# Kernel optimization log

Measured on AMD Instinct MI355X. Metric: run time of the kernel, lower is better.

Reference implementation:

```python
import math
import jax, jax.numpy as jnp
import numpy as np

H, KV, D = 16, 4, 128          # num_heads, num_kv_heads, head_dim
HID = 2048                      # hidden_size
ROPE_BASE = 1e6
EPS = 1e-6


def setup_inputs() -> dict:
    key = jax.random.key(0)
    ks = jax.random.split(key, 3)
    B, S = 2, 2048
    s = 0.02
    return {
        "x": jax.random.normal(ks[0], (B, S, HID), jnp.float32),
        "w_qkv": jax.random.normal(ks[1], (2 * H * D + 2 * KV * D, HID), jnp.float32) * s,
        "w_o": jax.random.normal(ks[2], (HID, H * D), jnp.float32) * s,
        "q_norm_w": jnp.ones((D,), jnp.float32),
        "q_norm_b": jnp.zeros((D,), jnp.float32),
        "k_norm_w": jnp.ones((D,), jnp.float32),
        "k_norm_b": jnp.zeros((D,), jnp.float32),
    }


def _layernorm(x, w, b):
    mu = jnp.mean(x, axis=-1, keepdims=True)
    xc = x - mu
    var = jnp.mean(xc * xc, axis=-1, keepdims=True)
    return xc * jax.lax.rsqrt(var + EPS) * w + b


def _rope(x, cos, sin):
    # x: [B, h, S, D]; cos/sin: [S, D/2]; interleaved real/imag pairs
    xr, xi = x[..., 0::2], x[..., 1::2]
    c, s = cos[None, None], sin[None, None]
    out = jnp.stack([xr * c - xi * s, xr * s + xi * c], axis=-1)
    return out.reshape(x.shape)


def reference(x, w_qkv, w_o, q_norm_w, q_norm_b, k_norm_w, k_norm_b):
    B, S, _ = x.shape
    qkv = x @ w_qkv.T                                  # [B,S,2*H*D+2*KV*D]
    qg, k, v = jnp.split(qkv, [2 * H * D, 2 * H * D + KV * D], axis=-1)
    q, gate = jnp.split(qg, 2, axis=-1)                # [B,S,H*D] each

    q = q.reshape(B, S, H, D).transpose(0, 2, 1, 3)    # [B,H,S,D]
    k = k.reshape(B, S, KV, D).transpose(0, 2, 1, 3)   # [B,KV,S,D]
    v = v.reshape(B, S, KV, D).transpose(0, 2, 1, 3)

    q = _layernorm(q, q_norm_w, q_norm_b)
    k = _layernorm(k, k_norm_w, k_norm_b)

    inv = 1.0 / (ROPE_BASE ** (jnp.arange(0, D, 2, dtype=jnp.float32) / D))
    freqs = jnp.outer(jnp.arange(S, dtype=jnp.float32), inv)  # [S, D/2]
    cos, sin = jnp.cos(freqs), jnp.sin(freqs)
    q = _rope(q, cos, sin)
    k = _rope(k, cos, sin)

    rep = H // KV
    k = jnp.repeat(k, rep, axis=1)                     # [B,H,S,D]
    v = jnp.repeat(v, rep, axis=1)

    scores = jnp.einsum('bhqd,bhkd->bhqk', q, k) / math.sqrt(D)
    causal = jnp.tril(jnp.ones((S, S), bool))
    scores = jnp.where(causal[None, None], scores, -jnp.inf)
    attn = jax.nn.softmax(scores, axis=-1)
    out = jnp.einsum('bhqk,bhkd->bhqd', attn, v)
    out = out.transpose(0, 2, 1, 3).reshape(B, S, H * D)
    out = out * jax.nn.sigmoid(gate)
    return out @ w_o.T
```

## Files before the change

kernel.cpp:

```cpp
#include <hip/hip_runtime.h>
#include <hip/hip_bf16.h>

typedef __bf16 bf16_t;
typedef __bf16 bf16x2 __attribute__((ext_vector_type(2)));
typedef __bf16 bf16x4v __attribute__((ext_vector_type(4)));
typedef __bf16 bf16x8 __attribute__((ext_vector_type(8)));
typedef float f32x4 __attribute__((ext_vector_type(4)));

#define LOG2E 1.4426950408889634f
#define QSCALE (0.08838834764831843f * 1.4426950408889634f)

__global__ __launch_bounds__(256) void cvt_all(const float* __restrict__ x, bf16_t* __restrict__ xb,
                                               const float* __restrict__ wq, bf16_t* __restrict__ wqb,
                                               const float* __restrict__ wo, bf16_t* __restrict__ wob,
                                               float* __restrict__ cosT, float* __restrict__ sinT) {
  int i = blockIdx.x * 256 + threadIdx.x;
  if (i < 5767168) {
    const float* in; bf16_t* out; int idx;
    if (i < 2097152)      { in = x;  out = xb;  idx = i; }
    else if (i < 4718592) { in = wq; out = wqb; idx = i - 2097152; }
    else                  { in = wo; out = wob; idx = i - 4718592; }
    float4 v = ((const float4*)in)[idx];
    bf16x4v o;
    o[0] = (__bf16)v.x; o[1] = (__bf16)v.y; o[2] = (__bf16)v.z; o[3] = (__bf16)v.w;
    *(bf16x4v*)(out + (size_t)idx * 4) = o;
  } else {
    int idx = i - 5767168;
    int s = idx >> 6, fi = idx & 63;
    float inv = __builtin_amdgcn_exp2f(-(float)fi * (19.931568569324174f / 64.0f));
    float f = (float)s * inv;
    cosT[idx] = cosf(f);
    sinT[idx] = sinf(f);
  }
}

template<int MI, int NI, typename OT>
__global__ __launch_bounds__(512) void gemm8p(const bf16_t* __restrict__ A,
                                              const bf16_t* __restrict__ B,
                                              OT* __restrict__ C,
                                              int M, int N, int K) {
  constexpr int BM = MI * 32;
  constexpr int BN = NI * 64;
  constexpr int NA = BM / 64;
  constexpr int NB = BN / 64;
  constexpr int ST = NA + NB;
  static_assert(MI == 8 || MI == 4, "banked phases assume MI in {4,8}");

  __shared__ bf16_t LA[2][BM * 64];
  __shared__ bf16_t LB[2][BN * 64];

  int nb = N / BN;
  int cpx = gridDim.x >> 3;
  int bid = blockIdx.x;
  int swz = (bid & 7) * cpx + (bid >> 3);
  int bm = swz / nb, bn = swz % nb;
  int m0 = bm * BM, n0 = bn * BN;
  int tid = threadIdx.x, lane = tid & 63, wv = tid >> 6;
  int wr = wv >> 2, wc = wv & 3, lr = lane & 15, g = lane >> 4;
  int T = K >> 6;

  auto stageI = [&](int kt, int bi, int s) {
    int k0 = kt << 6;
    if (s < NA) {
      int c = s * 512 + tid;
      int row = c >> 3, lc = (c & 7) ^ (row & 7);
      __builtin_amdgcn_global_load_lds(
          (const __attribute__((address_space(1))) void*)(A + (size_t)(m0 + row) * K + k0 + lc * 8),
          (__attribute__((address_space(3))) void*)&LA[bi][(s * 512 + wv * 64) * 8], 16, 0, 0);
    } else {
      int c = (s - NA) * 512 + tid;
      int row = c >> 3, lc = (c & 7) ^ (row & 7);
      __builtin_amdgcn_global_load_lds(
          (const __attribute__((address_space(1))) void*)(B + (size_t)(n0 + row) * K + k0 + lc * 8),
          (__attribute__((address_space(3))) void*)&LB[bi][((s - NA) * 512 + wv * 64) * 8], 16, 0, 0);
    }
  };

  f32x4 acc[MI][NI];
#pragma unroll
  for (int i = 0; i < MI; i++)
#pragma unroll
    for (int j = 0; j < NI; j++)
#pragma unroll
      for (int r = 0; r < 4; r++) acc[i][j][r] = 0.f;

#pragma unroll
  for (int s = 0; s < ST; s++) stageI(0, 0, s);
  asm volatile("s_waitcnt vmcnt(0)" ::: "memory");
  __builtin_amdgcn_s_barrier();
  asm volatile("" ::: "memory");

  int ofk0 = ((0 + g) ^ (lr & 7)) << 3;
  int ofk1 = ((4 + g) ^ (lr & 7)) << 3;
  int offA = (wr * (MI * 16) + lr) * 64;
  int offB = (wc * (NI * 16) + lr) * 64;

  for (int t = 0; t < T; t++) {
    int bi = t & 1, bo = bi ^ 1;
    const bf16_t* la = LA[bi];
    const bf16_t* lb = LB[bi];
    bool pre = (t + 1 < T);
    if (pre) {
#pragma unroll
      for (int s = 0; s < ST; s++) stageI(t + 1, bo, s);
    }

    bf16x8 bq0[NI], bq1[NI], afA[4], afB[4];
#pragma unroll
    for (int ni = 0; ni < NI; ni++) bq0[ni] = *(const bf16x8*)&lb[offB + ni * 1024 + ofk0];
#pragma unroll
    for (int i = 0; i < 4; i++) afA[i] = *(const bf16x8*)&la[offA + i * 1024 + ofk0];

    if constexpr (MI == 8) {
#pragma unroll
      for (int i = 0; i < 4; i++) afB[i] = *(const bf16x8*)&la[offA + (4 + i) * 1024 + ofk0];
#pragma unroll
      for (int i = 0; i < 4; i++)
#pragma unroll
        for (int ni = 0; ni < NI; ni++)
          acc[i][ni] = __builtin_amdgcn_mfma_f32_16x16x32_bf16(afA[i], bq0[ni], acc[i][ni], 0, 0, 0);
#pragma unroll
      for (int i = 0; i < 4; i++) afA[i] = *(const bf16x8*)&la[offA + i * 1024 + ofk1];
#pragma unroll
      for (int ni = 0; ni < NI; ni++) bq1[ni] = *(const bf16x8*)&lb[offB + ni * 1024 + ofk1];
#pragma unroll
      for (int i = 0; i < 4; i++)
#pragma unroll
        for (int ni = 0; ni < NI; ni++)
          acc[4 + i][ni] = __builtin_amdgcn_mfma_f32_16x16x32_bf16(afB[i], bq0[ni], acc[4 + i][ni], 0, 0, 0);
#pragma unroll
      for (int i = 0; i < 4; i++) afB[i] = *(const bf16x8*)&la[offA + (4 + i) * 1024 + ofk1];
#pragma unroll
      for (int i = 0; i < 4; i++)
#pragma unroll
        for (int ni = 0; ni < NI; ni++)
          acc[i][ni] = __builtin_amdgcn_mfma_f32_16x16x32_bf16(afA[i], bq1[ni], acc[i][ni], 0, 0, 0);
#pragma unroll
      for (int i = 0; i < 4; i++)
#pragma unroll
        for (int ni = 0; ni < NI; ni++)
          acc[4 + i][ni] = __builtin_amdgcn_mfma_f32_16x16x32_bf16(afB[i], bq1[ni], acc[4 + i][ni], 0, 0, 0);
    } else {
#pragma unroll
      for (int i = 0; i < 4; i++) afB[i] = *(const bf16x8*)&la[offA + i * 1024 + ofk1];
#pragma unroll
      for (int ni = 0; ni < NI; ni++) bq1[ni] = *(const bf16x8*)&lb[offB + ni * 1024 + ofk1];
#pragma unroll
      for (int i = 0; i < 4; i++)
#pragma unroll
        for (int ni = 0; ni < NI; ni++)
          acc[i][ni] = __builtin_amdgcn_mfma_f32_16x16x32_bf16(afA[i], bq0[ni], acc[i][ni], 0, 0, 0);
#pragma unroll
      for (int i = 0; i < 4; i++)
#pragma unroll
        for (int ni = 0; ni < NI; ni++)
          acc[i][ni] = __builtin_amdgcn_mfma_f32_16x16x32_bf16(afB[i], bq1[ni], acc[i][ni], 0, 0, 0);
    }

    if (pre) {
      asm volatile("s_waitcnt vmcnt(0) lgkmcnt(0)" ::: "memory");
      __builtin_amdgcn_s_barrier();
      asm volatile("" ::: "memory");
    }
  }

#pragma unroll
  for (int mi = 0; mi < MI; mi++)
#pragma unroll
    for (int ni = 0; ni < NI; ni++) {
      int m = m0 + wr * (MI * 16) + mi * 16 + g * 4;
      int n = n0 + wc * (NI * 16) + ni * 16 + lr;
#pragma unroll
      for (int r = 0; r < 4; r++) C[(size_t)(m + r) * N + n] = (OT)acc[mi][ni][r];
    }
}

__global__ __launch_bounds__(256) void ln_rope(const bf16_t* __restrict__ qkv,
                                               const float* __restrict__ qw, const float* __restrict__ qb,
                                               const float* __restrict__ kw, const float* __restrict__ kb,
                                               const float* __restrict__ cosT, const float* __restrict__ sinT,
                                               bf16_t* __restrict__ Qr, bf16_t* __restrict__ Kr) {
  int row = blockIdx.x;
  int b = row >> 11, s = row & 2047;
  int tid = threadIdx.x, gi = tid >> 4, li = tid & 15;
  const bf16_t* base = qkv + (size_t)row * 5120;
  float4 c4 = *(const float4*)(cosT + (s << 6) + (li << 2));
  float4 s4 = *(const float4*)(sinT + (s << 6) + (li << 2));
#pragma unroll
  for (int it = 0; it < 2; it++) {
    int head;
    if (it == 0) head = gi;
    else { if (gi >= 4) break; head = 16 + gi; }
    bool isq = (it == 0);
    int off = isq ? (head << 7) : (4096 + ((head - 16) << 7));
    bf16x8 xv = *(const bf16x8*)(base + off + (li << 3));
    float xf[8];
#pragma unroll
    for (int j = 0; j < 8; j++) xf[j] = (float)xv[j];
    float sum = 0.f;
#pragma unroll
    for (int j = 0; j < 8; j++) sum += xf[j];
#pragma unroll
    for (int m = 1; m < 16; m <<= 1) sum += __shfl_xor(sum, m);
    float mu = sum * 0.0078125f;
    float vs = 0.f;
#pragma unroll
    for (int j = 0; j < 8; j++) { xf[j] -= mu; vs += xf[j] * xf[j]; }
#pragma unroll
    for (int m = 1; m < 16; m <<= 1) vs += __shfl_xor(vs, m);
    float rs = rsqrtf(vs * 0.0078125f + 1e-6f);
    const float* w = isq ? qw : kw;
    const float* bb = isq ? qb : kb;
    float4 w0 = *(const float4*)(w + (li << 3));
    float4 w1 = *(const float4*)(w + (li << 3) + 4);
    float4 b0 = *(const float4*)(bb + (li << 3));
    float4 b1 = *(const float4*)(bb + (li << 3) + 4);
    float y[8];
    y[0] = xf[0] * rs * w0.x + b0.x; y[1] = xf[1] * rs * w0.y + b0.y;
    y[2] = xf[2] * rs * w0.z + b0.z; y[3] = xf[3] * rs * w0.w + b0.w;
    y[4] = xf[4] * rs * w1.x + b1.x; y[5] = xf[5] * rs * w1.y + b1.y;
    y[6] = xf[6] * rs * w1.z + b1.z; y[7] = xf[7] * rs * w1.w + b1.w;
    float cc[4] = { c4.x, c4.y, c4.z, c4.w };
    float ss[4] = { s4.x, s4.y, s4.z, s4.w };
    bf16x8 ov;
#pragma unroll
    for (int p = 0; p < 4; p++) {
      float o0 = y[2 * p] * cc[p] - y[2 * p + 1] * ss[p];
      float o1 = y[2 * p] * ss[p] + y[2 * p + 1] * cc[p];
      if (isq) { o0 *= QSCALE; o1 *= QSCALE; }
      ov[2 * p] = (__bf16)o0; ov[2 * p + 1] = (__bf16)o1;
    }
    size_t dst = isq ? ((((size_t)(b * 16 + head)) * 2048 + s) * 128 + (li << 3))
                     : ((((size_t)(b * 4 + (head - 16))) * 2048 + s) * 128 + (li << 3));
    *(bf16x8*)((isq ? Qr : Kr) + dst) = ov;
  }
}

__global__ __launch_bounds__(256) void vtrans(const bf16_t* __restrict__ qkv,
                                              bf16_t* __restrict__ Vt) {
  int bid = blockIdx.x;
  int sb = bid & 63, kv = (bid >> 6) & 3, b = bid >> 8;
  int s0 = sb << 5;
  __shared__ bf16_t T[128 * 33];
  int tid = threadIdx.x;
#pragma unroll
  for (int i = 0; i < 16; i++) {
    int idx = i * 256 + tid;
    int r = idx >> 7, d = idx & 127;
    T[d * 33 + r] = qkv[((size_t)(b * 2048 + s0 + r)) * 5120 + 4608 + (kv << 7) + d];
  }
  __syncthreads();
#pragma unroll
  for (int j = 0; j < 16; j++) {
    int idx = j * 256 + tid;
    int d = idx >> 5, sc = idx & 31;
    Vt[(((size_t)(b * 4 + kv)) * 128 + d) * 2048 + s0 + sc] = T[d * 33 + sc];
  }
}

__global__ __launch_bounds__(256, 3) void attn(const bf16_t* __restrict__ Qr,
                                               const bf16_t* __restrict__ Kr,
                                               const bf16_t* __restrict__ Vt,
                                               const bf16_t* __restrict__ qkv,
                                               bf16_t* __restrict__ ag) {
  __shared__ bf16_t Ks[2][32 * 128];
  __shared__ bf16_t Vs[2][128 * 32];
  int bid = blockIdx.x;
  int hb = bid & 31;
  int h = hb & 15, b = hb >> 4;
  int pr = bid >> 5;
  int kvh = h >> 2;
  int tid = threadIdx.x, lane = tid & 63, wv = tid >> 6;
  int lr = lane & 15, g = lane >> 4;
  int r0base = ((lr >> 2) << 3) + (lr & 3);

  const bf16_t* Kg = Kr + ((size_t)(b * 4 + kvh)) * 2048 * 128;
  const bf16_t* Vg = Vt + ((size_t)(b * 4 + kvh)) * 128 * 2048;

  auto stage = [&](int buf, int kv0) {
#pragma unroll
    for (int i = 0; i < 2; i++) {
      int c = i * 256 + tid;
      int row = c >> 4, lc = (c & 15) ^ (row & 15);
      __builtin_amdgcn_global_load_lds(
          (const __attribute__((address_space(1))) void*)(Kg + (size_t)(kv0 + row) * 128 + lc * 8),
          (__attribute__((address_space(3))) void*)&Ks[buf][c * 8], 16, 0, 0);
    }
#pragma unroll
    for (int i = 0; i < 2; i++) {
      int c = i * 256 + tid;
      int d = c >> 2, cv = (c & 3) ^ ((d >> 1) & 3);
      __builtin_amdgcn_global_load_lds(
          (const __attribute__((address_space(1))) void*)(Vg + (size_t)d * 2048 + kv0 + cv * 8),
          (__attribute__((address_space(3))) void*)&Vs[buf][c * 8], 16, 0, 0);
    }
  };

  auto sm = [&](const f32x4& s0, const f32x4& s1, int qrow, int kvabs, bool dia,
                float& mrun, float& lsp, bf16x8& pb, f32x4 (&oac)[8]) {
    float tt[8];
#pragma unroll
    for (int r = 0; r < 4; r++) { tt[r] = s0[r]; tt[4 + r] = s1[r]; }
    if (dia) {
#pragma unroll
      for (int r = 0; r < 4; r++) {
        if (kvabs + r > qrow)     tt[r]     = -1e30f;
        if (kvabs + 4 + r > qrow) tt[4 + r] = -1e30f;
      }
    }
    float lm = fmaxf(fmaxf(fmaxf(tt[0], tt[1]), tt[2]),
                     fmaxf(fmaxf(tt[3], tt[4]), fmaxf(fmaxf(tt[5], tt[6]), tt[7])));
    if (__all(lm <= mrun + 8.f)) {
      float ps = 0.f;
#pragma unroll
      for (int i = 0; i < 8; i++) {
        float pv = __builtin_amdgcn_exp2f(tt[i] - mrun);
        pb[i] = (__bf16)pv; ps += pv;
      }
      lsp += ps;
    } else {
      float pm = lm;
      pm = fmaxf(pm, __shfl_xor(pm, 16));
      pm = fmaxf(pm, __shfl_xor(pm, 32));
      float mnew = fmaxf(mrun, pm);
      float corr = __builtin_amdgcn_exp2f(mrun - mnew);
      float ps = 0.f;
#pragma unroll
      for (int i = 0; i < 8; i++) {
        float pv = __builtin_amdgcn_exp2f(tt[i] - mnew);
        pb[i] = (__bf16)pv; ps += pv;
      }
      lsp = lsp * corr + ps;
      mrun = mnew;
#pragma unroll
      for (int dt = 0; dt < 8; dt++)
#pragma unroll
        for (int r = 0; r < 4; r++) oac[dt][r] *= corr;
    }
  };

  for (int phase = 0; phase < 2; phase++) {
    int qb = phase ? (31 - pr) : pr;
    int qw0 = qb << 6;
    int qw = qw0 + (wv << 4);
    int qrow = qw + lr;
    int qmax = qw + 15;
    int nt = (qb + 1) << 1;

    const bf16_t* Qg = Qr + (((size_t)(b * 16 + h)) * 2048 + qrow) * 128;
    bf16x8 qf[4];
#pragma unroll
    for (int ds = 0; ds < 4; ds++) qf[ds] = *(const bf16x8*)(Qg + ds * 32 + g * 8);

    f32x4 oa[8];
#pragma unroll
    for (int i = 0; i < 8; i++)
#pragma unroll
      for (int r = 0; r < 4; r++) oa[i][r] = 0.f;
    float mrun = -1e30f, lsp = 0.f;

    stage(0, 0);
    asm volatile("s_waitcnt vmcnt(0)" ::: "memory");
    __builtin_amdgcn_s_barrier();
    asm volatile("" ::: "memory");
    for (int t = 0; t < nt; t++) {
      int cur = t & 1;
      if (t + 1 < nt) stage(cur ^ 1, (t + 1) << 5);
      int kvb = t << 5;
      if (kvb <= qmax) {
        const bf16_t* kb = Ks[cur];
        const bf16_t* vb = Vs[cur];
        int ra = r0base, rb2 = r0base + 4;
        bf16x8 a0[4], a1[4];
#pragma unroll
        for (int ds = 0; ds < 4; ds++) {
          a0[ds] = *(const bf16x8*)&kb[ra * 128 + (((ds * 4 + g) ^ (ra & 15)) << 3)];
          a1[ds] = *(const bf16x8*)&kb[rb2 * 128 + (((ds * 4 + g) ^ (rb2 & 15)) << 3)];
        }
        f32x4 s0, s1;
#pragma unroll
        for (int r = 0; r < 4; r++) { s0[r] = 0.f; s1[r] = 0.f; }
        __builtin_amdgcn_s_setprio(1);
#pragma unroll
        for (int ds = 0; ds < 4; ds++) {
          s0 = __builtin_amdgcn_mfma_f32_16x16x32_bf16(a0[ds], qf[ds], s0, 0, 0, 0);
          s1 = __builtin_amdgcn_mfma_f32_16x16x32_bf16(a1[ds], qf[ds], s1, 0, 0, 0);
        }
        __builtin_amdgcn_s_setprio(0);
        int kvabs = kvb + (g << 3);
        bool dia = (kvb + 31 > qw);
        bf16x8 pb;
        sm(s0, s1, qrow, kvabs, dia, mrun, lsp, pb, oa);
        __builtin_amdgcn_s_setprio(1);
#pragma unroll
        for (int dt = 0; dt < 8; dt++) {
          int d = dt * 16 + lr;
          bf16x8 va = *(const bf16x8*)&vb[d * 32 + ((g ^ ((d >> 1) & 3)) << 3)];
          oa[dt] = __builtin_amdgcn_mfma_f32_16x16x32_bf16(va, pb, oa[dt], 0, 0, 0);
        }
        __builtin_amdgcn_s_setprio(0);
      }
      asm volatile("s_waitcnt vmcnt(0) lgkmcnt(0)" ::: "memory");
      __builtin_amdgcn_s_barrier();
      asm volatile("" ::: "memory");
    }

    float ls = lsp + __shfl_xor(lsp, 16);
    ls += __shfl_xor(ls, 32);
    float invl = __builtin_amdgcn_rcpf(ls);

    size_t ob = ((size_t)b * 2048 + qrow) * 2048 + (h << 7);
    size_t gb = ((size_t)b * 2048 + qrow) * 5120 + 2048 + (h << 7);
#pragma unroll
    for (int dt = 0; dt < 8; dt++) {
      int d = dt * 16 + (g << 2);
      bf16x4v gt = *(const bf16x4v*)(qkv + gb + d);
      bf16x4v o;
#pragma unroll
      for (int r = 0; r < 4; r++)
        o[r] = (__bf16)(oa[dt][r] * invl *
                        __builtin_amdgcn_rcpf(1.f + __builtin_amdgcn_exp2f(-(float)gt[r] * LOG2E)));
      *(bf16x4v*)(ag + ob + d) = o;
    }
  }
}

extern "C" void kernel_launch(void* const* d_in, const int* in_sizes, int n_in,
                              void* d_out, int out_size, void* d_ws, size_t ws_size,
                              hipStream_t stream) {
  const float* x    = (const float*)d_in[0];
  const float* wqkv = (const float*)d_in[1];
  const float* wo   = (const float*)d_in[2];
  const float* qnw  = (const float*)d_in[3];
  const float* qnb  = (const float*)d_in[4];
  const float* knw  = (const float*)d_in[5];
  const float* knb  = (const float*)d_in[6];
  float* out = (float*)d_out;

  char* p = (char*)d_ws;
  bf16_t* xb  = (bf16_t*)p;
  bf16_t* ag  = xb;
  p += (size_t)16777216;
  bf16_t* wqb = (bf16_t*)p;
  bf16_t* Qr  = wqb;
  p += (size_t)20971520;
  bf16_t* wob = (bf16_t*)p; p += (size_t)8388608;
  bf16_t* qkv = (bf16_t*)p; p += (size_t)41943040;
  bf16_t* Kr  = (bf16_t*)p; p += (size_t)4194304;
  bf16_t* Vt  = (bf16_t*)p; p += (size_t)4194304;
  float* cosT = (float*)p;  p += (size_t)524288;
  float* sinT = (float*)p;  p += (size_t)524288;

  cvt_all<<<23040, 256, 0, stream>>>(x, xb, wqkv, wqb, wo, wob, cosT, sinT);

  gemm8p<8, 5, bf16_t><<<256, 512, 0, stream>>>(xb, wqb, qkv, 4096, 5120, 2048);

  ln_rope<<<4096, 256, 0, stream>>>(qkv, qnw, qnb, knw, knb, cosT, sinT, Qr, Kr);
  vtrans<<<512, 256, 0, stream>>>(qkv, Vt);

  attn<<<512, 256, 0, stream>>>(Qr, Kr, Vt, qkv, ag);

  gemm8p<4, 4, float><<<256, 512, 0, stream>>>(ag, wob, out, 4096, 2048, 2048);
}
```

Baseline: 231.5 us.

## Use single-buffered 128-row QKV GEMM with higher occupancy instead of double-buffered tile

```diff
diff --git a/kernel.cpp b/kernel.cpp
--- a/kernel.cpp
+++ b/kernel.cpp
@@ -34,6 +34,100 @@
   }
 }
 
+template<int NI, typename OT>
+__global__ __launch_bounds__(512, 4) void gemm4s(const bf16_t* __restrict__ A,
+                                                 const bf16_t* __restrict__ B,
+                                                 OT* __restrict__ C,
+                                                 int M, int N, int K) {
+  constexpr int BM = 128;
+  constexpr int BN = NI * 64;
+  constexpr int NA = 2;
+  constexpr int NB = NI;
+  constexpr int ST = NA + NB;
+
+  __shared__ bf16_t LA[BM * 64];
+  __shared__ bf16_t LB[BN * 64];
+
+  int nb = N / BN;
+  int cpx = gridDim.x >> 3;
+  int bid = blockIdx.x;
+  int swz = (bid & 7) * cpx + (bid >> 3);
+  int bm = swz / nb, bn = swz % nb;
+  int m0 = bm * BM, n0 = bn * BN;
+  int tid = threadIdx.x, lane = tid & 63, wv = tid >> 6;
+  int wr = wv >> 2, wc = wv & 3, lr = lane & 15, g = lane >> 4;
+  int T = K >> 6;
+
+  auto stageI = [&](int kt, int s) {
+    int k0 = kt << 6;
+    if (s < NA) {
+      int c = s * 512 + tid;
+      int row = c >> 3, lc = (c & 7) ^ (row & 7);
+      __builtin_amdgcn_global_load_lds(
+          (const __attribute__((address_space(1))) void*)(A + (size_t)(m0 + row) * K + k0 + lc * 8),
+          (__attribute__((address_space(3))) void*)&LA[(s * 512 + wv * 64) * 8], 16, 0, 0);
+    } else {
+      int c = (s - NA) * 512 + tid;
+      int row = c >> 3, lc = (c & 7) ^ (row & 7);
+      __builtin_amdgcn_global_load_lds(
+          (const __attribute__((address_space(1))) void*)(B + (size_t)(n0 + row) * K + k0 + lc * 8),
+          (__attribute__((address_space(3))) void*)&LB[((s - NA) * 512 + wv * 64) * 8], 16, 0, 0);
+    }
+  };
+
+  f32x4 acc[4][NI];
+#pragma unroll
+  for (int i = 0; i < 4; i++)
+#pragma unroll
+    for (int j = 0; j < NI; j++)
+#pragma unroll
+      for (int r = 0; r < 4; r++) acc[i][j][r] = 0.f;
+
+  int ofk0 = ((0 + g) ^ (lr & 7)) << 3;
+  int ofk1 = ((4 + g) ^ (lr & 7)) << 3;
+  int offA = (wr * 64 + lr) * 64;
+  int offB = (wc * (NI * 16) + lr) * 64;
+
+  for (int t = 0; t < T; t++) {
+#pragma unroll
+    for (int s = 0; s < ST; s++) stageI(t, s);
+    asm volatile("s_waitcnt vmcnt(0)" ::: "memory");
+    __builtin_amdgcn_s_barrier();
+    asm volatile("" ::: "memory");
+
+#pragma unroll
+    for (int ks = 0; ks < 2; ks++) {
+      const int ofk = ks ? ofk1 : ofk0;
+      bf16x8 bq[NI];
+#pragma unroll
+      for (int ni = 0; ni < NI; ni++) bq[ni] = *(const bf16x8*)&LB[offB + ni * 1024 + ofk];
+#pragma unroll
+      for (int i = 0; i < 4; i++) {
+        bf16x8 af = *(const bf16x8*)&LA[offA + i * 1024 + ofk];
+#pragma unroll
+        for (int ni = 0; ni < NI; ni++)
+          acc[i][ni] = __builtin_amdgcn_mfma_f32_16x16x32_bf16(af, bq[ni], acc[i][ni], 0, 0, 0);
+      }
+    }
+
+    if (t + 1 < T) {
+      asm volatile("s_waitcnt lgkmcnt(0)" ::: "memory");
+      __builtin_amdgcn_s_barrier();
+      asm volatile("" ::: "memory");
+    }
+  }
+
+#pragma unroll
+  for (int mi = 0; mi < 4; mi++)
+#pragma unroll
+    for (int ni = 0; ni < NI; ni++) {
+      int m = m0 + wr * 64 + mi * 16 + g * 4;
+      int n = n0 + wc * (NI * 16) + ni * 16 + lr;
+#pragma unroll
+      for (int r = 0; r < 4; r++) C[(size_t)(m + r) * N + n] = (OT)acc[mi][ni][r];
+    }
+}
+
 template<int MI, int NI, typename OT>
 __global__ __launch_bounds__(512) void gemm8p(const bf16_t* __restrict__ A,
                                               const bf16_t* __restrict__ B,
@@ -44,7 +138,6 @@
   constexpr int NA = BM / 64;
   constexpr int NB = BN / 64;
   constexpr int ST = NA + NB;
-  static_assert(MI == 8 || MI == 4, "banked phases assume MI in {4,8}");
 
   __shared__ bf16_t LA[2][BM * 64];
   __shared__ bf16_t LB[2][BN * 64];
@@ -105,56 +198,32 @@
       for (int s = 0; s < ST; s++) stageI(t + 1, bo, s);
     }
 
-    bf16x8 bq0[NI], bq1[NI], afA[4], afB[4];
+    bf16x8 bq0[NI], bq1[NI];
 #pragma unroll
     for (int ni = 0; ni < NI; ni++) bq0[ni] = *(const bf16x8*)&lb[offB + ni * 1024 + ofk0];
 #pragma unroll
-    for (int i = 0; i < 4; i++) afA[i] = *(const bf16x8*)&la[offA + i * 1024 + ofk0];
-
-    if constexpr (MI == 8) {
-#pragma unroll
-      for (int i = 0; i < 4; i++) afB[i] = *(const bf16x8*)&la[offA + (4 + i) * 1024 + ofk0];
+    for (int ni = 0; ni < NI; ni++) bq1[ni] = *(const bf16x8*)&lb[offB + ni * 1024 + ofk1];
+#pragma unroll
+    for (int q = 0; q < MI / 4; q++) {
+      bf16x8 af0[4], af1[4];
 #pragma unroll
       for (int i = 0; i < 4; i++)
+        af0[i] = *(const bf16x8*)&la[offA + (q * 4 + i) * 1024 + ofk0];
+#pragma unroll
+      for (int i = 0; i < 4; i++)
 #pragma unroll
         for (int ni = 0; ni < NI; ni++)
-          acc[i][ni] = __builtin_amdgcn_mfma_f32_16x16x32_bf16(afA[i], bq0[ni], acc[i][ni], 0, 0, 0);
-#pragma unroll
-      for (int i = 0; i < 4; i++) afA[i] = *(const bf16x8*)&la[offA + i * 1024 + ofk1];
-#pragma unroll
-      for (int ni = 0; ni < NI; ni++) bq1[ni] = *(const bf16x8*)&lb[offB + ni * 1024 + ofk1];
+          acc[q * 4 + i][ni] =
+              __builtin_amdgcn_mfma_f32_16x16x32_bf16(af0[i], bq0[ni], acc[q * 4 + i][ni], 0, 0, 0);
 #pragma unroll
       for (int i = 0; i < 4; i++)
+        af1[i] = *(const bf16x8*)&la[offA + (q * 4 + i) * 1024 + ofk1];
+#pragma unroll
+      for (int i = 0; i < 4; i++)
 #pragma unroll
         for (int ni = 0; ni < NI; ni++)
-          acc[4 + i][ni] = __builtin_amdgcn_mfma_f32_16x16x32_bf16(afB[i], bq0[ni], acc[4 + i][ni], 0, 0, 0);
-#pragma unroll
-      for (int i = 0; i < 4; i++) afB[i] = *(const bf16x8*)&la[offA + (4 + i) * 1024 + ofk1];
-#pragma unroll
-      for (int i = 0; i < 4; i++)
-#pragma unroll
-        for (int ni = 0; ni < NI; ni++)
-          acc[i][ni] = __builtin_amdgcn_mfma_f32_16x16x32_bf16(afA[i], bq1[ni], acc[i][ni], 0, 0, 0);
-#pragma unroll
-      for (int i = 0; i < 4; i++)
-#pragma unroll
-        for (int ni = 0; ni < NI; ni++)
-          acc[4 + i][ni] = __builtin_amdgcn_mfma_f32_16x16x32_bf16(afB[i], bq1[ni], acc[4 + i][ni], 0, 0, 0);
-    } else {
-#pragma unroll
-      for (int i = 0; i < 4; i++) afB[i] = *(const bf16x8*)&la[offA + i * 1024 + ofk1];
-#pragma unroll
-      for (int ni = 0; ni < NI; ni++) bq1[ni] = *(const bf16x8*)&lb[offB + ni * 1024 + ofk1];
-#pragma unroll
-      for (int i = 0; i < 4; i++)
-#pragma unroll
-        for (int ni = 0; ni < NI; ni++)
-          acc[i][ni] = __builtin_amdgcn_mfma_f32_16x16x32_bf16(afA[i], bq0[ni], acc[i][ni], 0, 0, 0);
-#pragma unroll
-      for (int i = 0; i < 4; i++)
-#pragma unroll
-        for (int ni = 0; ni < NI; ni++)
-          acc[i][ni] = __builtin_amdgcn_mfma_f32_16x16x32_bf16(afB[i], bq1[ni], acc[i][ni], 0, 0, 0);
+          acc[q * 4 + i][ni] =
+              __builtin_amdgcn_mfma_f32_16x16x32_bf16(af1[i], bq1[ni], acc[q * 4 + i][ni], 0, 0, 0);
     }
 
     if (pre) {
@@ -453,7 +522,7 @@
 
   cvt_all<<<23040, 256, 0, stream>>>(x, xb, wqkv, wqb, wo, wob, cosT, sinT);
 
-  gemm8p<8, 5, bf16_t><<<256, 512, 0, stream>>>(xb, wqb, qkv, 4096, 5120, 2048);
+  gemm4s<5, bf16_t><<<512, 512, 0, stream>>>(xb, wqb, qkv, 4096, 5120, 2048);
 
   ln_rope<<<4096, 256, 0, stream>>>(qkv, qnw, qnb, knw, knb, cosT, sinT, Qr, Kr);
   vtrans<<<512, 256, 0, stream>>>(qkv, Vt);
```

Result: faster. 224.6 us (-3.0%).
